# Kernel optimization log

Measured on AMD Instinct MI355X. Metric: run time of the kernel, lower is better.

## Reference

```python
import jax, jax.numpy as jnp
import numpy as np

BETA = 0.1
PAD = 0
NORMALIZE_LENGTH = True
B, T, V = 64, 512, 512


def setup_inputs() -> dict:
    key = jax.random.key(0)
    k1, k2, k3, k4 = jax.random.split(key, 4)
    inp = jax.random.normal(k1, (B, T, V), dtype=jnp.float32)
    target = jax.random.randint(k2, (B, T), 0, V, dtype=jnp.int64 if jax.config.read('jax_enable_x64') else jnp.int32)
    length = jax.random.randint(k3, (B,), 1, T).astype(jnp.float32)
    # confusion matrix: rows over last axis normalized to sum to 1 (probabilities)
    m = jax.random.uniform(k4, (V, V, V), dtype=jnp.float32)
    matric = m / m.sum(axis=-1, keepdims=True)
    return {"input": inp, "target": target, "length": length, "matric": matric}


def reference(input, target, length, matric):
    b, t, v = input.shape
    n = b * t
    # previous-token targets (shifted right, first position = 0)
    forth = jnp.concatenate([jnp.zeros((b, 1), target.dtype), target[:, :-1]], axis=1).reshape(-1)
    tgt = target.reshape(-1)
    ignore = tgt == PAD                     # [N]
    total = ignore.sum().astype(input.dtype)
    log_prob = jax.nn.log_softmax(input.reshape(n, v), axis=-1)  # [N, V]
    # per-utterance smoothing 1 - (1-beta)^(1/L), broadcast over time
    smoothing = 1.0 - jnp.power(1.0 - BETA, 1.0 / length)        # [B]
    smoothing = jnp.broadcast_to(smoothing[:, None], (b, t)).reshape(-1)  # [N]
    # gather V-length confusion rows indexed by (prev, cur) token pair
    weight = smoothing[:, None] * matric[forth, tgt, :]          # [N, V]
    src = 1.0 - weight.sum(axis=1)                               # [N]
    weight = weight.at[jnp.arange(n), tgt].set(src)              # scatter diag mass
    denom = total if NORMALIZE_LENGTH else jnp.asarray(b, input.dtype)
    loss = jnp.where(ignore[:, None], 0.0, -weight * log_prob).sum() / denom
    return loss
```

## Files before the change

kernel.cpp:

```cpp
#include <hip/hip_runtime.h>


#define T_DIM 512
#define V_DIM 512
#define LN_0_9 (-0.1053605157f)

__global__ __launch_bounds__(256) void pwl_main_kernel(
    const float* __restrict__ input,
    const int*   __restrict__ target,
    const float* __restrict__ length,
    const float* __restrict__ matric,
    float*       __restrict__ acc,
    int N)
{
    const int lane = threadIdx.x & 63;
    const int wave = threadIdx.x >> 6;
    const int n = blockIdx.x * 4 + wave;

    __shared__ float    s_num;
    __shared__ unsigned s_cnt;
    if (threadIdx.x == 0) { s_num = 0.0f; s_cnt = 0u; }
    __syncthreads();

    if (n < N) {
        const int t = target[n];
        if (t == 0) {
            if (lane == 0) atomicAdd(&s_cnt, 1u);
        } else {
            const int b  = n / T_DIM;
            const int tp = n % T_DIM;
            const int f  = (tp == 0) ? 0 : target[n - 1];

            const float4* xrow = (const float4*)(input + (size_t)n * V_DIM);
            const float4 x0 = xrow[lane];
            const float4 x1 = xrow[lane + 64];

            float mx = fmaxf(fmaxf(fmaxf(x0.x, x0.y), fmaxf(x0.z, x0.w)),
                             fmaxf(fmaxf(x1.x, x1.y), fmaxf(x1.z, x1.w)));
            #pragma unroll
            for (int off = 32; off > 0; off >>= 1)
                mx = fmaxf(mx, __shfl_xor(mx, off, 64));

            float se = expf(x0.x - mx) + expf(x0.y - mx) + expf(x0.z - mx) + expf(x0.w - mx)
                     + expf(x1.x - mx) + expf(x1.y - mx) + expf(x1.z - mx) + expf(x1.w - mx);
            #pragma unroll
            for (int off = 32; off > 0; off >>= 1)
                se += __shfl_xor(se, off, 64);
            const float lse = mx + logf(se);

            const float4* mrow = (const float4*)(matric + ((size_t)f * V_DIM + t) * V_DIM);
            const float4 m0 = mrow[lane];
            const float4 m1 = mrow[lane + 64];

            float dot = m0.x * x0.x + m0.y * x0.y + m0.z * x0.z + m0.w * x0.w
                      + m1.x * x1.x + m1.y * x1.y + m1.z * x1.z + m1.w * x1.w;
            float rs  = m0.x + m0.y + m0.z + m0.w + m1.x + m1.y + m1.z + m1.w;

            float Mt = 0.0f, xt = 0.0f;
            {
                const float mv0[4] = {m0.x, m0.y, m0.z, m0.w};
                const float xv0[4] = {x0.x, x0.y, x0.z, x0.w};
                const float mv1[4] = {m1.x, m1.y, m1.z, m1.w};
                const float xv1[4] = {x1.x, x1.y, x1.z, x1.w};
                int d0 = t - 4 * lane;
                if ((unsigned)d0 < 4u) { Mt = mv0[d0]; xt = xv0[d0]; }
                int d1 = t - (256 + 4 * lane);
                if ((unsigned)d1 < 4u) { Mt = mv1[d1]; xt = xv1[d1]; }
            }

            #pragma unroll
            for (int off = 32; off > 0; off >>= 1) {
                dot += __shfl_xor(dot, off, 64);
                rs  += __shfl_xor(rs,  off, 64);
                Mt  += __shfl_xor(Mt,  off, 64);
                xt  += __shfl_xor(xt,  off, 64);
            }

            if (lane == 0) {
                const float L = length[b];
                const float s = 1.0f - expf(LN_0_9 / L);
                const float src = 1.0f - s * rs;
                const float contrib = s * (dot - lse * rs) + (src - s * Mt) * (xt - lse);
                atomicAdd(&s_num, -contrib);
            }
        }
    }

    __syncthreads();
    if (threadIdx.x == 0) {
        atomicAdd(&acc[0], s_num);
        atomicAdd((unsigned*)acc + 1, s_cnt);
    }
}

__global__ void pwl_final_kernel(const float* __restrict__ acc, float* __restrict__ out)
{
    const unsigned cnt = ((const unsigned*)acc)[1];
    out[0] = acc[0] / (float)cnt;
}

extern "C" void kernel_launch(void* const* d_in, const int* in_sizes, int n_in,
                              void* d_out, int out_size, void* d_ws, size_t ws_size,
                              hipStream_t stream) {
    const float* input  = (const float*)d_in[0];
    const int*   target = (const int*)  d_in[1];
    const float* length = (const float*)d_in[2];
    const float* matric = (const float*)d_in[3];
    float* out = (float*)d_out;
    float* acc = (float*)d_ws;

    const int N = in_sizes[1];

    hipMemsetAsync(acc, 0, 2 * sizeof(float), stream);

    const int blocks = (N + 3) / 4;
    pwl_main_kernel<<<blocks, 256, 0, stream>>>(input, target, length, matric, acc, N);
    pwl_final_kernel<<<1, 1, 0, stream>>>(acc, out);
}
```

Baseline: 779.8 us.

## Process four rows per wave and replace atomics with two-stage reduction

Each wave now handles four rows strided by the total wave count, prefetching their targets up front, and accumulates its partial loss and ignore count in registers. The shared-memory and global atomics are replaced by per-wave partial sums written to the workspace and summed by a 256-thread final kernel, which also removes the memset launch. The diagonal element is now fetched with a single lane shuffle instead of two extra butterfly reductions. This trims launch and atomic overhead and reduction work, but gives a quarter as many blocks, so fewer independent waves are available to hide memory latency in this bandwidth-bound kernel.

After: 630.2 us. 19.2% less time.

```diff
diff --git a/kernel.cpp b/kernel.cpp
--- a/kernel.cpp
+++ b/kernel.cpp
@@ -5,98 +5,127 @@
 #define V_DIM 512
 #define LN_0_9 (-0.1053605157f)
 
+__device__ __forceinline__ float pick4(float4 v, int k) {
+    const float lo = (k & 1) ? v.y : v.x;
+    const float hi = (k & 1) ? v.w : v.z;
+    return (k & 2) ? hi : lo;
+}
+
 __global__ __launch_bounds__(256) void pwl_main_kernel(
     const float* __restrict__ input,
     const int*   __restrict__ target,
     const float* __restrict__ length,
     const float* __restrict__ matric,
-    float*       __restrict__ acc,
-    int N)
+    float*       __restrict__ ws,
+    int N, int nwaves)
 {
     const int lane = threadIdx.x & 63;
     const int wave = threadIdx.x >> 6;
-    const int n = blockIdx.x * 4 + wave;
+    const int wgid = blockIdx.x * 4 + wave;
 
-    __shared__ float    s_num;
-    __shared__ unsigned s_cnt;
-    if (threadIdx.x == 0) { s_num = 0.0f; s_cnt = 0u; }
-    __syncthreads();
-
-    if (n < N) {
-        const int t = target[n];
-        if (t == 0) {
-            if (lane == 0) atomicAdd(&s_cnt, 1u);
+    int ts[4], fs[4];
+    #pragma unroll
+    for (int p = 0; p < 4; ++p) {
+        const int n = wgid + p * nwaves;
+        if (n < N) {
+            ts[p] = target[n];
+            const int tp = n & (T_DIM - 1);
+            fs[p] = (tp == 0) ? 0 : target[n - 1];
         } else {
-            const int b  = n / T_DIM;
-            const int tp = n % T_DIM;
-            const int f  = (tp == 0) ? 0 : target[n - 1];
-
-            const float4* xrow = (const float4*)(input + (size_t)n * V_DIM);
-            const float4 x0 = xrow[lane];
-            const float4 x1 = xrow[lane + 64];
-
-            float mx = fmaxf(fmaxf(fmaxf(x0.x, x0.y), fmaxf(x0.z, x0.w)),
-                             fmaxf(fmaxf(x1.x, x1.y), fmaxf(x1.z, x1.w)));
-            #pragma unroll
-            for (int off = 32; off > 0; off >>= 1)
-                mx = fmaxf(mx, __shfl_xor(mx, off, 64));
-
-            float se = expf(x0.x - mx) + expf(x0.y - mx) + expf(x0.z - mx) + expf(x0.w - mx)
-                     + expf(x1.x - mx) + expf(x1.y - mx) + expf(x1.z - mx) + expf(x1.w - mx);
-            #pragma unroll
-            for (int off = 32; off > 0; off >>= 1)
-                se += __shfl_xor(se, off, 64);
-            const float lse = mx + logf(se);
-
-            const float4* mrow = (const float4*)(matric + ((size_t)f * V_DIM + t) * V_DIM);
-            const float4 m0 = mrow[lane];
-            const float4 m1 = mrow[lane + 64];
-
-            float dot = m0.x * x0.x + m0.y * x0.y + m0.z * x0.z + m0.w * x0.w
-                      + m1.x * x1.x + m1.y * x1.y + m1.z * x1.z + m1.w * x1.w;
-            float rs  = m0.x + m0.y + m0.z + m0.w + m1.x + m1.y + m1.z + m1.w;
-
-            float Mt = 0.0f, xt = 0.0f;
-            {
-                const float mv0[4] = {m0.x, m0.y, m0.z, m0.w};
-                const float xv0[4] = {x0.x, x0.y, x0.z, x0.w};
-                const float mv1[4] = {m1.x, m1.y, m1.z, m1.w};
-                const float xv1[4] = {x1.x, x1.y, x1.z, x1.w};
-                int d0 = t - 4 * lane;
-                if ((unsigned)d0 < 4u) { Mt = mv0[d0]; xt = xv0[d0]; }
-                int d1 = t - (256 + 4 * lane);
-                if ((unsigned)d1 < 4u) { Mt = mv1[d1]; xt = xv1[d1]; }
-            }
-
-            #pragma unroll
-            for (int off = 32; off > 0; off >>= 1) {
-                dot += __shfl_xor(dot, off, 64);
-                rs  += __shfl_xor(rs,  off, 64);
-                Mt  += __shfl_xor(Mt,  off, 64);
-                xt  += __shfl_xor(xt,  off, 64);
-            }
-
-            if (lane == 0) {
-                const float L = length[b];
-                const float s = 1.0f - expf(LN_0_9 / L);
-                const float src = 1.0f - s * rs;
-                const float contrib = s * (dot - lse * rs) + (src - s * Mt) * (xt - lse);
-                atomicAdd(&s_num, -contrib);
-            }
+            ts[p] = -1;
+            fs[p] = 0;
         }
     }
 
-    __syncthreads();
-    if (threadIdx.x == 0) {
-        atomicAdd(&acc[0], s_num);
-        atomicAdd((unsigned*)acc + 1, s_cnt);
+    float acc_sum = 0.0f;
+    int   acc_cnt = 0;
+
+    #pragma unroll
+    for (int p = 0; p < 4; ++p) {
+        const int n = wgid + p * nwaves;
+        const int t = ts[p];
+        if (t < 0) continue;
+        if (t == 0) { acc_cnt++; continue; }
+
+        const int b = n / T_DIM;
+        const int f = fs[p];
+
+        const float4* xrow = (const float4*)(input + (size_t)n * V_DIM);
+        const float4 x0 = xrow[lane];
+        const float4 x1 = xrow[lane + 64];
+
+        const float4* mrow = (const float4*)(matric + ((size_t)f * V_DIM + t) * V_DIM);
+        const float4 m0 = mrow[lane];
+        const float4 m1 = mrow[lane + 64];
+
+        float mx = fmaxf(fmaxf(fmaxf(x0.x, x0.y), fmaxf(x0.z, x0.w)),
+                         fmaxf(fmaxf(x1.x, x1.y), fmaxf(x1.z, x1.w)));
+        #pragma unroll
+        for (int off = 32; off > 0; off >>= 1)
+            mx = fmaxf(mx, __shfl_xor(mx, off, 64));
+
+        float se = expf(x0.x - mx) + expf(x0.y - mx) + expf(x0.z - mx) + expf(x0.w - mx)
+                 + expf(x1.x - mx) + expf(x1.y - mx) + expf(x1.z - mx) + expf(x1.w - mx);
+        #pragma unroll
+        for (int off = 32; off > 0; off >>= 1)
+            se += __shfl_xor(se, off, 64);
+        const float lse = mx + logf(se);
+
+        float dot = m0.x * x0.x + m0.y * x0.y + m0.z * x0.z + m0.w * x0.w
+                  + m1.x * x1.x + m1.y * x1.y + m1.z * x1.z + m1.w * x1.w;
+        float rs  = m0.x + m0.y + m0.z + m0.w + m1.x + m1.y + m1.z + m1.w;
+        #pragma unroll
+        for (int off = 32; off > 0; off >>= 1) {
+            dot += __shfl_xor(dot, off, 64);
+            rs  += __shfl_xor(rs,  off, 64);
+        }
+
+        const int  k       = t & 3;
+        const int  srcLane = (t >> 2) & 63;
+        const bool hiHalf  = (t >= 256);
+        const float cm = hiHalf ? pick4(m1, k) : pick4(m0, k);
+        const float cx = hiHalf ? pick4(x1, k) : pick4(x0, k);
+        const float Mt = __shfl(cm, srcLane, 64);
+        const float xt = __shfl(cx, srcLane, 64);
+
+        const float L = length[b];
+        const float s = 1.0f - expf(LN_0_9 / L);
+        const float src = 1.0f - s * rs;
+        const float contrib = s * (dot - lse * rs) + (src - s * Mt) * (xt - lse);
+        acc_sum += contrib;
+    }
+
+    if (lane == 0) {
+        ws[wgid]          = acc_sum;
+        ws[nwaves + wgid] = (float)acc_cnt;
     }
 }
 
-__global__ void pwl_final_kernel(const float* __restrict__ acc, float* __restrict__ out)
+__global__ __launch_bounds__(256) void pwl_final_kernel(
+    const float* __restrict__ ws, float* __restrict__ out, int nwaves)
 {
-    const unsigned cnt = ((const unsigned*)acc)[1];
-    out[0] = acc[0] / (float)cnt;
+    const int lane = threadIdx.x & 63;
+    const int wave = threadIdx.x >> 6;
+
+    float s = 0.0f, c = 0.0f;
+    for (int i = threadIdx.x; i < nwaves; i += 256) {
+        s += ws[i];
+        c += ws[nwaves + i];
+    }
+    #pragma unroll
+    for (int off = 32; off > 0; off >>= 1) {
+        s += __shfl_xor(s, off, 64);
+        c += __shfl_xor(c, off, 64);
+    }
+
+    __shared__ float ss[4], sc[4];
+    if (lane == 0) { ss[wave] = s; sc[wave] = c; }
+    __syncthreads();
+    if (threadIdx.x == 0) {
+        float S = ss[0] + ss[1] + ss[2] + ss[3];
+        float C = sc[0] + sc[1] + sc[2] + sc[3];
+        out[0] = -S / C;
+    }
 }
 
 extern "C" void kernel_launch(void* const* d_in, const int* in_sizes, int n_in,
@@ -107,13 +136,13 @@
     const float* length = (const float*)d_in[2];
     const float* matric = (const float*)d_in[3];
     float* out = (float*)d_out;
-    float* acc = (float*)d_ws;
+    float* ws  = (float*)d_ws;
 
     const int N = in_sizes[1];
 
-    hipMemsetAsync(acc, 0, 2 * sizeof(float), stream);
+    const int blocks = (N + 15) / 16;
+    const int nwaves = blocks * 4;
 
-    const int blocks = (N + 3) / 4;
-    pwl_main_kernel<<<blocks, 256, 0, stream>>>(input, target, length, matric, acc, N);
-    pwl_final_kernel<<<1, 1, 0, stream>>>(acc, out);
+    pwl_main_kernel<<<blocks, 256, 0, stream>>>(input, target, length, matric, ws, N, nwaves);
+    pwl_final_kernel<<<1, 256, 0, stream>>>(ws, out, nwaves);
 }
```
